# Kernel optimization log

Hardware: AMD Instinct MI355X
Metric: run time of the kernel (lower is better)

Reference implementation:

```python
import jax, jax.numpy as jnp
import numpy as np

N_QUBITS = 4
N_LAYERS = 3
H_IMG = 512

# ---------- 4-qubit statevector simulator, batched over P patches ----------

def _apply_1q(psi, U, w):
    # shared 2x2 gate U on wire w; psi: (P,2,2,2,2)
    psi = jnp.moveaxis(psi, 1 + w, -1)
    psi = jnp.einsum('ij,...j->...i', U, psi)
    return jnp.moveaxis(psi, -1, 1 + w)

def _apply_1q_batched(psi, U, w):
    # per-patch gate U: (P,2,2)
    psi = jnp.moveaxis(psi, 1 + w, -1)
    psi = jnp.einsum('pij,p...j->p...i', U, psi)
    return jnp.moveaxis(psi, -1, 1 + w)

def _apply_cnot(psi, c, t):
    psi = jnp.moveaxis(psi, (1 + c, 1 + t), (-2, -1))
    top = psi[..., 0:1, :]
    bot = psi[..., 1:2, ::-1]  # X on target when control=1
    psi = jnp.concatenate([top, bot], axis=-2)
    return jnp.moveaxis(psi, (-2, -1), (1 + c, 1 + t))

def _rx(theta):
    # AngleEmbedding default rotation='X'; theta: (P,) -> (P,2,2)
    h = theta * 0.5
    c = jnp.cos(h).astype(jnp.complex64)
    s = (-1j * jnp.sin(h)).astype(jnp.complex64)
    return jnp.stack([jnp.stack([c, s], -1), jnp.stack([s, c], -1)], -2)

def _rot(phi, theta, omega):
    # PennyLane Rot = RZ(omega) RY(theta) RZ(phi)
    c = jnp.cos(theta * 0.5)
    s = jnp.sin(theta * 0.5)
    em = jnp.exp(-0.5j * (phi + omega))
    ep = jnp.exp(0.5j * (phi + omega))
    fm = jnp.exp(0.5j * (phi - omega))
    fp = jnp.exp(-0.5j * (phi - omega))
    row0 = jnp.stack([em * c, -fm * s])
    row1 = jnp.stack([fp * s, ep * c])
    return jnp.stack([row0, row1]).astype(jnp.complex64)

def _qsim(inputs, weights):
    # inputs: (P,4) angles; weights: (3,4,3) Rot params -> (P,4) PauliZ expvals
    P = inputs.shape[0]
    psi = jnp.zeros((P, 2, 2, 2, 2), jnp.complex64).at[:, 0, 0, 0, 0].set(1.0)
    for w in range(N_QUBITS):
        psi = _apply_1q_batched(psi, _rx(inputs[:, w]), w)
    for l in range(N_LAYERS):
        for w in range(N_QUBITS):
            psi = _apply_1q(psi, _rot(weights[l, w, 0], weights[l, w, 1], weights[l, w, 2]), w)
        r = (l % (N_QUBITS - 1)) + 1  # StronglyEntanglingLayers default ranges
        for w in range(N_QUBITS):
            psi = _apply_cnot(psi, w, (w + r) % N_QUBITS)
    probs = psi.real ** 2 + psi.imag ** 2  # (P,2,2,2,2)
    ez = []
    for w in range(N_QUBITS):
        axes = tuple(a for a in range(1, 5) if a != 1 + w)
        p = probs.sum(axes)  # (P,2)
        ez.append(p[:, 0] - p[:, 1])
    return jnp.stack(ez, -1)  # (P,4)

def _qconv(x, q_weights):
    img = x[0, 0]  # (H,W)
    a = img[:-1, :-1]; b = img[:-1, 1:]; c = img[1:, :-1]; d = img[1:, 1:]
    Hm, Wm = a.shape
    patches = jnp.stack([a, b, c, d], -1).reshape(-1, 4)  # row-major 2x2 flatten
    ez = _qsim(patches, q_weights)  # (P,4)
    return ez.reshape(Hm, Wm, 4).transpose(2, 0, 1)[None]  # (1,4,Hm,Wm)

# ---------- classical layers ----------

def _conv(x, w, b):
    y = jax.lax.conv_general_dilated(x, w, (1, 1), 'VALID',
                                     dimension_numbers=('NCHW', 'OIHW', 'NCHW'))
    return y + b[None, :, None, None]

def _maxpool2(x):
    return jax.lax.reduce_window(x, -jnp.inf, jax.lax.max,
                                 (1, 1, 2, 2), (1, 1, 2, 2), 'VALID')

def _adaptive_max(x, out):
    H, W = x.shape[-2], x.shape[-1]
    rows = []
    for i in range(out):
        si, ei = (i * H) // out, -(-((i + 1) * H) // out)
        cols = []
        for j in range(out):
            sj, ej = (j * W) // out, -(-((j + 1) * W) // out)
            cols.append(x[..., si:ei, sj:ej].max((-2, -1)))
        rows.append(jnp.stack(cols, -1))
    return jnp.stack(rows, -2)


def setup_inputs() -> dict:
    key = jax.random.key(0)
    ks = jax.random.split(key, 10)
    x = jax.random.normal(ks[0], (1, 1, H_IMG, H_IMG), jnp.float32)
    q_weights = jax.random.uniform(ks[1], (N_LAYERS, N_QUBITS, 3), jnp.float32,
                                   0.0, 2.0 * np.pi)
    conv2_w = jax.random.normal(ks[2], (20, 4, 5, 5), jnp.float32) * 0.05
    conv2_b = jax.random.normal(ks[3], (20,), jnp.float32) * 0.05
    conv3_w = jax.random.normal(ks[4], (40, 20, 3, 3), jnp.float32) * 0.05
    conv3_b = jax.random.normal(ks[5], (40,), jnp.float32) * 0.05
    fc1_w = jax.random.normal(ks[6], (64, 640), jnp.float32) * 0.05
    fc1_b = jax.random.normal(ks[7], (64,), jnp.float32) * 0.05
    fc2_w = jax.random.normal(ks[8], (10, 64), jnp.float32) * 0.05
    fc2_b = jax.random.normal(ks[9], (10,), jnp.float32) * 0.05
    return {'x': x, 'q_weights': q_weights,
            'conv2_w': conv2_w, 'conv2_b': conv2_b,
            'conv3_w': conv3_w, 'conv3_b': conv3_b,
            'fc1_w': fc1_w, 'fc1_b': fc1_b,
            'fc2_w': fc2_w, 'fc2_b': fc2_b}


def reference(x, q_weights, conv2_w, conv2_b, conv3_w, conv3_b,
              fc1_w, fc1_b, fc2_w, fc2_b):
    h = _maxpool2(jax.nn.sigmoid(_qconv(x, q_weights)))        # (1,4,255,255)
    h = _maxpool2(jax.nn.relu(_conv(h, conv2_w, conv2_b)))      # (1,20,125,125)
    h = _adaptive_max(jax.nn.relu(_conv(h, conv3_w, conv3_b)), 4)  # (1,40,4,4)
    h = h.reshape(-1, 640)
    h = jax.nn.relu(h @ fc1_w.T + fc1_b)
    return h @ fc2_w.T + fc2_b  # (1,10)
```

## Files before the change

kernel.cpp:

```cpp
#include <hip/hip_runtime.h>
#include <math.h>

#define IMG 512
#define QO  255
#define QP  256
#define C2H 125
#define C2S 128
#define C3H 123
#define C3S 128

template<int M_>
__device__ inline void rot_regs(float2* a, float2 U00, float2 U01, float2 U10, float2 U11) {
    #pragma unroll
    for (int s = 0; s < 16; ++s) {
        if (!(s & M_)) {
            float2 a0 = a[s], a1 = a[s | M_];
            a[s]      = make_float2(U00.x*a0.x - U00.y*a0.y + U01.x*a1.x - U01.y*a1.y,
                                    U00.x*a0.y + U00.y*a0.x + U01.x*a1.y + U01.y*a1.x);
            a[s | M_] = make_float2(U10.x*a0.x - U10.y*a0.y + U11.x*a1.x - U11.y*a1.y,
                                    U10.x*a0.y + U10.y*a0.x + U11.x*a1.y + U11.y*a1.x);
        }
    }
}
template<int MC, int MT>
__device__ inline void cnot_regs(float2* a) {
    #pragma unroll
    for (int s = 0; s < 16; ++s) {
        if ((s & MC) && !(s & MT)) {
            float2 t = a[s]; a[s] = a[s | MT]; a[s | MT] = t;
        }
    }
}
__device__ inline void rot_gate_params(float phi, float th, float om,
                                       float2& U00, float2& U01, float2& U10, float2& U11) {
    float ch, sh, ca, sa, cb, sb;
    __sincosf(0.5f * th, &sh, &ch);
    __sincosf(0.5f * (phi + om), &sa, &ca);
    __sincosf(0.5f * (phi - om), &sb, &cb);
    U00 = make_float2( ca*ch, -sa*ch);
    U01 = make_float2(-cb*sh, -sb*sh);
    U10 = make_float2( cb*sh, -sb*sh);
    U11 = make_float2( ca*ch,  sa*ch);
}

__global__ void build_M(const float* __restrict__ qw, float2* __restrict__ Mout) {
    int t = threadIdx.x;
    if (t >= 16) return;
    float2 a[16];
    #pragma unroll
    for (int s = 0; s < 16; ++s) a[s] = make_float2(s == t ? 1.f : 0.f, 0.f);

    float2 U00, U01, U10, U11;
#define ROTG(L, W) rot_gate_params(qw[((L)*4+(W))*3+0], qw[((L)*4+(W))*3+1], qw[((L)*4+(W))*3+2], U00,U01,U10,U11); \
                   rot_regs<(1 << (3-(W)))>(a, U00, U01, U10, U11);
    ROTG(0,0) ROTG(0,1) ROTG(0,2) ROTG(0,3)
    cnot_regs<8,4>(a); cnot_regs<4,2>(a); cnot_regs<2,1>(a); cnot_regs<1,8>(a);
    ROTG(1,0) ROTG(1,1) ROTG(1,2) ROTG(1,3)
    cnot_regs<8,2>(a); cnot_regs<4,1>(a); cnot_regs<2,8>(a); cnot_regs<1,4>(a);
    ROTG(2,0) ROTG(2,1) ROTG(2,2) ROTG(2,3)
    cnot_regs<8,1>(a); cnot_regs<4,8>(a); cnot_regs<2,4>(a); cnot_regs<1,2>(a);
#undef ROTG

    int pc = __popc(t) & 3;
    #pragma unroll
    for (int row = 0; row < 16; ++row) {
        float2 v = a[row], o;
        if      (pc == 0) o = v;
        else if (pc == 1) o = make_float2( v.y, -v.x);
        else if (pc == 2) o = make_float2(-v.x, -v.y);
        else              o = make_float2(-v.y,  v.x);
        Mout[row * 16 + t] = o;
    }
}

__global__ __launch_bounds__(256) void qconv_pool(const float* __restrict__ img,
                                                  const float2* __restrict__ M2,
                                                  float* __restrict__ out) {
    int gid = blockIdx.x * 256 + threadIdx.x;
    if (gid >= QO * QO) return;
    int i = gid / QO, j = gid - i * QO;
    int r0 = 2 * i, c0 = 2 * j;

    float cs[3][3], sn[3][3];
    #pragma unroll
    for (int rr = 0; rr < 3; ++rr)
        #pragma unroll
        for (int cc = 0; cc < 3; ++cc) {
            float v = img[(r0 + rr) * IMG + c0 + cc];
            __sincosf(0.5f * v, &sn[rr][cc], &cs[rr][cc]);
        }

    float mx0 = -1e30f, mx1 = -1e30f, mx2 = -1e30f, mx3 = -1e30f;

    #pragma unroll
    for (int pr = 0; pr < 2; ++pr) {
        #pragma unroll
        for (int pc = 0; pc < 2; ++pc) {
            float c0v = cs[pr][pc],     s0 = sn[pr][pc];
            float c1v = cs[pr][pc+1],   s1 = sn[pr][pc+1];
            float c2v = cs[pr+1][pc],   s2 = sn[pr+1][pc];
            float c3v = cs[pr+1][pc+1], s3 = sn[pr+1][pc+1];
            float t01[4] = {c0v*c1v, c0v*s1, s0*c1v, s0*s1};
            float t23[4] = {c2v*c3v, c2v*s3, s2*c3v, s2*s3};
            float a[16];
            #pragma unroll
            for (int k = 0; k < 16; ++k) a[k] = t01[k >> 2] * t23[k & 3];

            float e0 = 0.f, e1 = 0.f, e2 = 0.f, e3 = 0.f;
            #pragma unroll 4
            for (int rw = 0; rw < 16; ++rw) {
                float re = 0.f, im = 0.f;
                #pragma unroll
                for (int k = 0; k < 16; ++k) {
                    float2 m = M2[rw * 16 + k];
                    re = fmaf(m.x, a[k], re);
                    im = fmaf(m.y, a[k], im);
                }
                float pp = fmaf(re, re, im * im);
                e0 += (rw & 8) ? -pp : pp;
                e1 += (rw & 4) ? -pp : pp;
                e2 += (rw & 2) ? -pp : pp;
                e3 += (rw & 1) ? -pp : pp;
            }
            mx0 = fmaxf(mx0, e0);
            mx1 = fmaxf(mx1, e1);
            mx2 = fmaxf(mx2, e2);
            mx3 = fmaxf(mx3, e3);
        }
    }

    int o = i * QP + j;
    out[0 * QP * QP + o] = 1.f / (1.f + __expf(-mx0));
    out[1 * QP * QP + o] = 1.f / (1.f + __expf(-mx1));
    out[2 * QP * QP + o] = 1.f / (1.f + __expf(-mx2));
    out[3 * QP * QP + o] = 1.f / (1.f + __expf(-mx3));
}

__global__ __launch_bounds__(256) void conv2_pool(const float* __restrict__ in,
                                                  const float* __restrict__ w,
                                                  const float* __restrict__ b,
                                                  float* __restrict__ out) {
    int oc = blockIdx.y;
    int sp = blockIdx.x * 256 + threadIdx.x;
    if (sp >= C2H * C2H) return;
    int i = sp / C2H, j = sp - i * C2H;
    const float* wb = w + oc * 100;

    float a00 = 0.f, a01 = 0.f, a10 = 0.f, a11 = 0.f;
    #pragma unroll
    for (int ic = 0; ic < 4; ++ic) {
        const float* ip = in + ic * QP * QP + (2 * i) * QP + 2 * j;
        float win[6][6];
        #pragma unroll
        for (int y = 0; y < 6; ++y) {
            #pragma unroll
            for (int h = 0; h < 3; ++h) {
                float2 v = *(const float2*)(ip + y * QP + 2 * h);
                win[y][2*h]   = v.x;
                win[y][2*h+1] = v.y;
            }
        }
        #pragma unroll
        for (int ky = 0; ky < 5; ++ky) {
            #pragma unroll
            for (int kx = 0; kx < 5; ++kx) {
                float wv = wb[ic * 25 + ky * 5 + kx];
                a00 = fmaf(win[ky][kx],     wv, a00);
                a01 = fmaf(win[ky][kx+1],   wv, a01);
                a10 = fmaf(win[ky+1][kx],   wv, a10);
                a11 = fmaf(win[ky+1][kx+1], wv, a11);
            }
        }
    }
    float m = fmaxf(fmaxf(a00, a01), fmaxf(a10, a11));
    out[oc * C2H * C2S + i * C2S + j] = fmaxf(m + b[oc], 0.f);
}

__global__ __launch_bounds__(256) void conv3_k(const float* __restrict__ in,
                                               const float* __restrict__ w,
                                               const float* __restrict__ b,
                                               float* __restrict__ out) {
    int og = blockIdx.y;
    int sp = blockIdx.x * 256 + threadIdx.x;
    if (sp >= C3H * C3H) return;
    int y = sp / C3H, x = sp - y * C3H;
    int oc0 = og * 4;
    const float* wb = w + oc0 * 180;

    float acc0 = 0.f, acc1 = 0.f, acc2 = 0.f, acc3 = 0.f;
    #pragma unroll
    for (int ic = 0; ic < 20; ++ic) {
        const float* ip = in + ic * C2H * C2S + y * C2S + x;
        float v[3][3];
        #pragma unroll
        for (int ky = 0; ky < 3; ++ky)
            #pragma unroll
            for (int kx = 0; kx < 3; ++kx)
                v[ky][kx] = ip[ky * C2S + kx];
        #pragma unroll
        for (int kk = 0; kk < 9; ++kk) {
            float iv = v[kk / 3][kk % 3];
            acc0 = fmaf(iv, wb[          ic * 9 + kk], acc0);
            acc1 = fmaf(iv, wb[180     + ic * 9 + kk], acc1);
            acc2 = fmaf(iv, wb[360     + ic * 9 + kk], acc2);
            acc3 = fmaf(iv, wb[540     + ic * 9 + kk], acc3);
        }
    }
    int o = y * C3S + x;
    out[(oc0 + 0) * C3H * C3S + o] = fmaxf(acc0 + b[oc0 + 0], 0.f);
    out[(oc0 + 1) * C3H * C3S + o] = fmaxf(acc1 + b[oc0 + 1], 0.f);
    out[(oc0 + 2) * C3H * C3S + o] = fmaxf(acc2 + b[oc0 + 2], 0.f);
    out[(oc0 + 3) * C3H * C3S + o] = fmaxf(acc3 + b[oc0 + 3], 0.f);
}

__global__ void amax_k(const float* __restrict__ in, float* __restrict__ out) {
    int ob = blockIdx.x;
    int oc = ob >> 4, bi = (ob >> 2) & 3, bj = ob & 3;
    int y0 = (bi * C3H) >> 2, y1 = ((bi + 1) * C3H + 3) >> 2;
    int x0 = (bj * C3H) >> 2, x1 = ((bj + 1) * C3H + 3) >> 2;
    int ny = y1 - y0, nx = x1 - x0, tot = ny * nx;
    float m = -1e30f;
    for (int e = threadIdx.x; e < tot; e += 64) {
        int yy = e / nx, xx = e - yy * nx;
        m = fmaxf(m, in[oc * C3H * C3S + (y0 + yy) * C3S + x0 + xx]);
    }
    #pragma unroll
    for (int o = 32; o > 0; o >>= 1) m = fmaxf(m, __shfl_down(m, o, 64));
    if (threadIdx.x == 0) out[ob] = m;
}

__global__ void fc_k(const float* __restrict__ h, const float* __restrict__ w1,
                     const float* __restrict__ b1, const float* __restrict__ w2,
                     const float* __restrict__ b2, float* __restrict__ out) {
    __shared__ float hh[640];
    __shared__ float h1[64];
    int t = threadIdx.x;
    for (int e = t; e < 640; e += 256) hh[e] = h[e];
    __syncthreads();

    int r = t >> 2, q = t & 3;
    const float4* wr = (const float4*)(w1 + r * 640 + q * 160);
    const float*  hp = hh + q * 160;
    float acc = 0.f;
    #pragma unroll 4
    for (int n = 0; n < 40; ++n) {
        float4 wv = wr[n];
        acc = fmaf(wv.x, hp[n*4+0], acc);
        acc = fmaf(wv.y, hp[n*4+1], acc);
        acc = fmaf(wv.z, hp[n*4+2], acc);
        acc = fmaf(wv.w, hp[n*4+3], acc);
    }
    acc += __shfl_xor(acc, 1, 64);
    acc += __shfl_xor(acc, 2, 64);
    if (q == 0) h1[r] = fmaxf(acc + b1[r], 0.f);
    __syncthreads();

    if (t < 10) {
        float o = b2[t];
        #pragma unroll 8
        for (int n = 0; n < 64; ++n) o = fmaf(h1[n], w2[t * 64 + n], o);
        out[t] = o;
    }
}

extern "C" void kernel_launch(void* const* d_in, const int* in_sizes, int n_in,
                              void* d_out, int out_size, void* d_ws, size_t ws_size,
                              hipStream_t stream) {
    const float* x   = (const float*)d_in[0];
    const float* qw  = (const float*)d_in[1];
    const float* c2w = (const float*)d_in[2];
    const float* c2b = (const float*)d_in[3];
    const float* c3w = (const float*)d_in[4];
    const float* c3b = (const float*)d_in[5];
    const float* f1w = (const float*)d_in[6];
    const float* f1b = (const float*)d_in[7];
    const float* f2w = (const float*)d_in[8];
    const float* f2b = (const float*)d_in[9];
    float* out = (float*)d_out;

    float*  wsf   = (float*)d_ws;
    float2* M     = (float2*)d_ws;
    float*  qout  = wsf + 512;
    float*  c2out = qout + 4 * QP * QP;
    float*  c3out = c2out + 20 * C2H * C2S;
    float*  am    = c3out + 40 * C3H * C3S;

    build_M<<<1, 64, 0, stream>>>(qw, M);
    qconv_pool<<<(QO * QO + 255) / 256, 256, 0, stream>>>(x, M, qout);
    conv2_pool<<<dim3((C2H * C2H + 255) / 256, 20), 256, 0, stream>>>(qout, c2w, c2b, c2out);
    conv3_k<<<dim3((C3H * C3H + 255) / 256, 10), 256, 0, stream>>>(c2out, c3w, c3b, c3out);
    amax_k<<<640, 64, 0, stream>>>(c3out, am);
    fc_k<<<1, 256, 0, stream>>>(am, f1w, f1b, f2w, f2b, out);
}
```

Baseline: 137.7 us.

## Fuse gate-matrix build into qconv, fuse adaptive max into conv3, split pool rows

The 16x16 circuit matrix is now built per block into shared memory inside qconv_pool, which removes the separate build_M launch and the global reads of M. Each pooled qconv output is now computed by two threads, one per pooling row, combined with a lane shuffle. That doubles parallelism and lowers per-thread work. The adaptive max pool is fused into conv3 using shared and global integer atomicMax on non-negative floats, so the conv3 output is never written to memory and the amax launch goes away. The cost is redundant matrix construction in every block, extra atomics, and zeroing of the pooled buffer inside conv2.

```diff
diff --git a/kernel.cpp b/kernel.cpp
--- a/kernel.cpp
+++ b/kernel.cpp
@@ -7,7 +7,6 @@
 #define C2H 125
 #define C2S 128
 #define C3H 123
-#define C3S 128
 
 template<int M_>
 __device__ inline void rot_regs(float2* a, float2 U00, float2 U01, float2 U10, float2 U11) {
@@ -43,47 +42,48 @@
     U11 = make_float2( ca*ch,  sa*ch);
 }
 
-__global__ void build_M(const float* __restrict__ qw, float2* __restrict__ Mout) {
-    int t = threadIdx.x;
-    if (t >= 16) return;
-    float2 a[16];
-    #pragma unroll
-    for (int s = 0; s < 16; ++s) a[s] = make_float2(s == t ? 1.f : 0.f, 0.f);
-
-    float2 U00, U01, U10, U11;
+__global__ __launch_bounds__(256) void qconv_pool(const float* __restrict__ img,
+                                                  const float* __restrict__ qw,
+                                                  float* __restrict__ out) {
+    __shared__ float2 Ms[256];
+    int tid = threadIdx.x;
+
+    if (tid < 16) {
+        float2 a[16];
+        #pragma unroll
+        for (int s = 0; s < 16; ++s) a[s] = make_float2(s == tid ? 1.f : 0.f, 0.f);
+        float2 U00, U01, U10, U11;
 #define ROTG(L, W) rot_gate_params(qw[((L)*4+(W))*3+0], qw[((L)*4+(W))*3+1], qw[((L)*4+(W))*3+2], U00,U01,U10,U11); \
                    rot_regs<(1 << (3-(W)))>(a, U00, U01, U10, U11);
-    ROTG(0,0) ROTG(0,1) ROTG(0,2) ROTG(0,3)
-    cnot_regs<8,4>(a); cnot_regs<4,2>(a); cnot_regs<2,1>(a); cnot_regs<1,8>(a);
-    ROTG(1,0) ROTG(1,1) ROTG(1,2) ROTG(1,3)
-    cnot_regs<8,2>(a); cnot_regs<4,1>(a); cnot_regs<2,8>(a); cnot_regs<1,4>(a);
-    ROTG(2,0) ROTG(2,1) ROTG(2,2) ROTG(2,3)
-    cnot_regs<8,1>(a); cnot_regs<4,8>(a); cnot_regs<2,4>(a); cnot_regs<1,2>(a);
+        ROTG(0,0) ROTG(0,1) ROTG(0,2) ROTG(0,3)
+        cnot_regs<8,4>(a); cnot_regs<4,2>(a); cnot_regs<2,1>(a); cnot_regs<1,8>(a);
+        ROTG(1,0) ROTG(1,1) ROTG(1,2) ROTG(1,3)
+        cnot_regs<8,2>(a); cnot_regs<4,1>(a); cnot_regs<2,8>(a); cnot_regs<1,4>(a);
+        ROTG(2,0) ROTG(2,1) ROTG(2,2) ROTG(2,3)
+        cnot_regs<8,1>(a); cnot_regs<4,8>(a); cnot_regs<2,4>(a); cnot_regs<1,2>(a);
 #undef ROTG
-
-    int pc = __popc(t) & 3;
-    #pragma unroll
-    for (int row = 0; row < 16; ++row) {
-        float2 v = a[row], o;
-        if      (pc == 0) o = v;
-        else if (pc == 1) o = make_float2( v.y, -v.x);
-        else if (pc == 2) o = make_float2(-v.x, -v.y);
-        else              o = make_float2(-v.y,  v.x);
-        Mout[row * 16 + t] = o;
-    }
-}
-
-__global__ __launch_bounds__(256) void qconv_pool(const float* __restrict__ img,
-                                                  const float2* __restrict__ M2,
-                                                  float* __restrict__ out) {
-    int gid = blockIdx.x * 256 + threadIdx.x;
-    if (gid >= QO * QO) return;
-    int i = gid / QO, j = gid - i * QO;
-    int r0 = 2 * i, c0 = 2 * j;
-
-    float cs[3][3], sn[3][3];
-    #pragma unroll
-    for (int rr = 0; rr < 3; ++rr)
+        int pc4 = __popc(tid) & 3;
+        #pragma unroll
+        for (int row = 0; row < 16; ++row) {
+            float2 v = a[row], o;
+            if      (pc4 == 0) o = v;
+            else if (pc4 == 1) o = make_float2( v.y, -v.x);
+            else if (pc4 == 2) o = make_float2(-v.x, -v.y);
+            else               o = make_float2(-v.y,  v.x);
+            Ms[row * 16 + tid] = o;
+        }
+    }
+    __syncthreads();
+
+    int gid = blockIdx.x * 256 + tid;
+    int pid = gid >> 1, p = gid & 1;
+    if (pid >= QO * QO) return;
+    int i = pid / QO, j = pid - i * QO;
+    int r0 = 2 * i + p, c0 = 2 * j;
+
+    float cs[2][3], sn[2][3];
+    #pragma unroll
+    for (int rr = 0; rr < 2; ++rr)
         #pragma unroll
         for (int cc = 0; cc < 3; ++cc) {
             float v = img[(r0 + rr) * IMG + c0 + cc];
@@ -93,53 +93,61 @@
     float mx0 = -1e30f, mx1 = -1e30f, mx2 = -1e30f, mx3 = -1e30f;
 
     #pragma unroll
-    for (int pr = 0; pr < 2; ++pr) {
-        #pragma unroll
-        for (int pc = 0; pc < 2; ++pc) {
-            float c0v = cs[pr][pc],     s0 = sn[pr][pc];
-            float c1v = cs[pr][pc+1],   s1 = sn[pr][pc+1];
-            float c2v = cs[pr+1][pc],   s2 = sn[pr+1][pc];
-            float c3v = cs[pr+1][pc+1], s3 = sn[pr+1][pc+1];
-            float t01[4] = {c0v*c1v, c0v*s1, s0*c1v, s0*s1};
-            float t23[4] = {c2v*c3v, c2v*s3, s2*c3v, s2*s3};
-            float a[16];
-            #pragma unroll
-            for (int k = 0; k < 16; ++k) a[k] = t01[k >> 2] * t23[k & 3];
-
-            float e0 = 0.f, e1 = 0.f, e2 = 0.f, e3 = 0.f;
-            #pragma unroll 4
-            for (int rw = 0; rw < 16; ++rw) {
-                float re = 0.f, im = 0.f;
-                #pragma unroll
-                for (int k = 0; k < 16; ++k) {
-                    float2 m = M2[rw * 16 + k];
-                    re = fmaf(m.x, a[k], re);
-                    im = fmaf(m.y, a[k], im);
-                }
-                float pp = fmaf(re, re, im * im);
-                e0 += (rw & 8) ? -pp : pp;
-                e1 += (rw & 4) ? -pp : pp;
-                e2 += (rw & 2) ? -pp : pp;
-                e3 += (rw & 1) ? -pp : pp;
-            }
-            mx0 = fmaxf(mx0, e0);
-            mx1 = fmaxf(mx1, e1);
-            mx2 = fmaxf(mx2, e2);
-            mx3 = fmaxf(mx3, e3);
-        }
-    }
-
-    int o = i * QP + j;
-    out[0 * QP * QP + o] = 1.f / (1.f + __expf(-mx0));
-    out[1 * QP * QP + o] = 1.f / (1.f + __expf(-mx1));
-    out[2 * QP * QP + o] = 1.f / (1.f + __expf(-mx2));
-    out[3 * QP * QP + o] = 1.f / (1.f + __expf(-mx3));
+    for (int pc = 0; pc < 2; ++pc) {
+        float c0v = cs[0][pc],   s0 = sn[0][pc];
+        float c1v = cs[0][pc+1], s1 = sn[0][pc+1];
+        float c2v = cs[1][pc],   s2 = sn[1][pc];
+        float c3v = cs[1][pc+1], s3 = sn[1][pc+1];
+        float t01[4] = {c0v*c1v, c0v*s1, s0*c1v, s0*s1};
+        float t23[4] = {c2v*c3v, c2v*s3, s2*c3v, s2*s3};
+        float a[16];
+        #pragma unroll
+        for (int k = 0; k < 16; ++k) a[k] = t01[k >> 2] * t23[k & 3];
+
+        float e0 = 0.f, e1 = 0.f, e2 = 0.f, e3 = 0.f;
+        #pragma unroll 4
+        for (int rw = 0; rw < 16; ++rw) {
+            float re = 0.f, im = 0.f;
+            #pragma unroll
+            for (int k = 0; k < 16; ++k) {
+                float2 m = Ms[rw * 16 + k];
+                re = fmaf(m.x, a[k], re);
+                im = fmaf(m.y, a[k], im);
+            }
+            float pp = fmaf(re, re, im * im);
+            e0 += (rw & 8) ? -pp : pp;
+            e1 += (rw & 4) ? -pp : pp;
+            e2 += (rw & 2) ? -pp : pp;
+            e3 += (rw & 1) ? -pp : pp;
+        }
+        mx0 = fmaxf(mx0, e0);
+        mx1 = fmaxf(mx1, e1);
+        mx2 = fmaxf(mx2, e2);
+        mx3 = fmaxf(mx3, e3);
+    }
+
+    mx0 = fmaxf(mx0, __shfl_xor(mx0, 1, 64));
+    mx1 = fmaxf(mx1, __shfl_xor(mx1, 1, 64));
+    mx2 = fmaxf(mx2, __shfl_xor(mx2, 1, 64));
+    mx3 = fmaxf(mx3, __shfl_xor(mx3, 1, 64));
+
+    if (p == 0) {
+        int o = i * QP + j;
+        out[0 * QP * QP + o] = 1.f / (1.f + __expf(-mx0));
+        out[1 * QP * QP + o] = 1.f / (1.f + __expf(-mx1));
+        out[2 * QP * QP + o] = 1.f / (1.f + __expf(-mx2));
+        out[3 * QP * QP + o] = 1.f / (1.f + __expf(-mx3));
+    }
 }
 
 __global__ __launch_bounds__(256) void conv2_pool(const float* __restrict__ in,
                                                   const float* __restrict__ w,
                                                   const float* __restrict__ b,
-                                                  float* __restrict__ out) {
+                                                  float* __restrict__ out,
+                                                  float* __restrict__ am) {
+    if (blockIdx.x == 0 && blockIdx.y == 0) {
+        for (int e = threadIdx.x; e < 640; e += 256) am[e] = 0.f;
+    }
     int oc = blockIdx.y;
     int sp = blockIdx.x * 256 + threadIdx.x;
     if (sp >= C2H * C2H) return;
@@ -176,57 +184,68 @@
     out[oc * C2H * C2S + i * C2S + j] = fmaxf(m + b[oc], 0.f);
 }
 
-__global__ __launch_bounds__(256) void conv3_k(const float* __restrict__ in,
-                                               const float* __restrict__ w,
-                                               const float* __restrict__ b,
-                                               float* __restrict__ out) {
-    int og = blockIdx.y;
+__global__ __launch_bounds__(256) void conv3_amax(const float* __restrict__ in,
+                                                  const float* __restrict__ w,
+                                                  const float* __restrict__ b,
+                                                  int* __restrict__ am) {
+    __shared__ int bm[64];
+    int og = blockIdx.y, oc0 = og * 4;
+    if (threadIdx.x < 64) bm[threadIdx.x] = 0;
+    __syncthreads();
+
     int sp = blockIdx.x * 256 + threadIdx.x;
-    if (sp >= C3H * C3H) return;
-    int y = sp / C3H, x = sp - y * C3H;
-    int oc0 = og * 4;
-    const float* wb = w + oc0 * 180;
-
-    float acc0 = 0.f, acc1 = 0.f, acc2 = 0.f, acc3 = 0.f;
-    #pragma unroll
-    for (int ic = 0; ic < 20; ++ic) {
-        const float* ip = in + ic * C2H * C2S + y * C2S + x;
-        float v[3][3];
-        #pragma unroll
-        for (int ky = 0; ky < 3; ++ky)
-            #pragma unroll
-            for (int kx = 0; kx < 3; ++kx)
-                v[ky][kx] = ip[ky * C2S + kx];
-        #pragma unroll
-        for (int kk = 0; kk < 9; ++kk) {
-            float iv = v[kk / 3][kk % 3];
-            acc0 = fmaf(iv, wb[          ic * 9 + kk], acc0);
-            acc1 = fmaf(iv, wb[180     + ic * 9 + kk], acc1);
-            acc2 = fmaf(iv, wb[360     + ic * 9 + kk], acc2);
-            acc3 = fmaf(iv, wb[540     + ic * 9 + kk], acc3);
-        }
-    }
-    int o = y * C3S + x;
-    out[(oc0 + 0) * C3H * C3S + o] = fmaxf(acc0 + b[oc0 + 0], 0.f);
-    out[(oc0 + 1) * C3H * C3S + o] = fmaxf(acc1 + b[oc0 + 1], 0.f);
-    out[(oc0 + 2) * C3H * C3S + o] = fmaxf(acc2 + b[oc0 + 2], 0.f);
-    out[(oc0 + 3) * C3H * C3S + o] = fmaxf(acc3 + b[oc0 + 3], 0.f);
-}
-
-__global__ void amax_k(const float* __restrict__ in, float* __restrict__ out) {
-    int ob = blockIdx.x;
-    int oc = ob >> 4, bi = (ob >> 2) & 3, bj = ob & 3;
-    int y0 = (bi * C3H) >> 2, y1 = ((bi + 1) * C3H + 3) >> 2;
-    int x0 = (bj * C3H) >> 2, x1 = ((bj + 1) * C3H + 3) >> 2;
-    int ny = y1 - y0, nx = x1 - x0, tot = ny * nx;
-    float m = -1e30f;
-    for (int e = threadIdx.x; e < tot; e += 64) {
-        int yy = e / nx, xx = e - yy * nx;
-        m = fmaxf(m, in[oc * C3H * C3S + (y0 + yy) * C3S + x0 + xx]);
-    }
-    #pragma unroll
-    for (int o = 32; o > 0; o >>= 1) m = fmaxf(m, __shfl_down(m, o, 64));
-    if (threadIdx.x == 0) out[ob] = m;
+    if (sp < C3H * C3H) {
+        int y = sp / C3H, x = sp - y * C3H;
+        const float* wb = w + oc0 * 180;
+
+        float acc0 = 0.f, acc1 = 0.f, acc2 = 0.f, acc3 = 0.f;
+        #pragma unroll
+        for (int ic = 0; ic < 20; ++ic) {
+            const float* ip = in + ic * C2H * C2S + y * C2S + x;
+            float v[3][3];
+            #pragma unroll
+            for (int ky = 0; ky < 3; ++ky)
+                #pragma unroll
+                for (int kx = 0; kx < 3; ++kx)
+                    v[ky][kx] = ip[ky * C2S + kx];
+            #pragma unroll
+            for (int kk = 0; kk < 9; ++kk) {
+                float iv = v[kk / 3][kk % 3];
+                acc0 = fmaf(iv, wb[      ic * 9 + kk], acc0);
+                acc1 = fmaf(iv, wb[180 + ic * 9 + kk], acc1);
+                acc2 = fmaf(iv, wb[360 + ic * 9 + kk], acc2);
+                acc3 = fmaf(iv, wb[540 + ic * 9 + kk], acc3);
+            }
+        }
+        acc0 = fmaxf(acc0 + b[oc0 + 0], 0.f);
+        acc1 = fmaxf(acc1 + b[oc0 + 1], 0.f);
+        acc2 = fmaxf(acc2 + b[oc0 + 2], 0.f);
+        acc3 = fmaxf(acc3 + b[oc0 + 3], 0.f);
+
+        const int bs[4] = {0, 30, 61, 92};
+        const int be[4] = {31, 62, 93, 123};
+        #pragma unroll
+        for (int yb = 0; yb < 4; ++yb) {
+            if (y >= bs[yb] && y < be[yb]) {
+                #pragma unroll
+                for (int xb = 0; xb < 4; ++xb) {
+                    if (x >= bs[xb] && x < be[xb]) {
+                        int bin = yb * 4 + xb;
+                        atomicMax(&bm[0 * 16 + bin], __float_as_int(acc0));
+                        atomicMax(&bm[1 * 16 + bin], __float_as_int(acc1));
+                        atomicMax(&bm[2 * 16 + bin], __float_as_int(acc2));
+                        atomicMax(&bm[3 * 16 + bin], __float_as_int(acc3));
+                    }
+                }
+            }
+        }
+    }
+    __syncthreads();
+    if (threadIdx.x < 64) {
+        int v = bm[threadIdx.x];
+        if (v != 0)
+            atomicMax(&am[(oc0 + (threadIdx.x >> 4)) * 16 + (threadIdx.x & 15)], v);
+    }
 }
 
 __global__ void fc_k(const float* __restrict__ h, const float* __restrict__ w1,
@@ -278,17 +297,13 @@
     const float* f2b = (const float*)d_in[9];
     float* out = (float*)d_out;
 
-    float*  wsf   = (float*)d_ws;
-    float2* M     = (float2*)d_ws;
-    float*  qout  = wsf + 512;
-    float*  c2out = qout + 4 * QP * QP;
-    float*  c3out = c2out + 20 * C2H * C2S;
-    float*  am    = c3out + 40 * C3H * C3S;
-
-    build_M<<<1, 64, 0, stream>>>(qw, M);
-    qconv_pool<<<(QO * QO + 255) / 256, 256, 0, stream>>>(x, M, qout);
-    conv2_pool<<<dim3((C2H * C2H + 255) / 256, 20), 256, 0, stream>>>(qout, c2w, c2b, c2out);
-    conv3_k<<<dim3((C3H * C3H + 255) / 256, 10), 256, 0, stream>>>(c2out, c3w, c3b, c3out);
-    amax_k<<<640, 64, 0, stream>>>(c3out, am);
+    float* wsf   = (float*)d_ws;
+    float* qout  = wsf;
+    float* c2out = qout + 4 * QP * QP;
+    float* am    = c2out + 20 * C2H * C2S;
+
+    qconv_pool<<<(2 * QO * QO + 255) / 256, 256, 0, stream>>>(x, qw, qout);
+    conv2_pool<<<dim3((C2H * C2H + 255) / 256, 20), 256, 0, stream>>>(qout, c2w, c2b, c2out, am);
+    conv3_amax<<<dim3((C3H * C3H + 255) / 256, 10), 256, 0, stream>>>(c2out, c3w, c3b, (int*)am);
     fc_k<<<1, 256, 0, stream>>>(am, f1w, f1b, f2w, f2b, out);
 }
```

Result: slower. 142.3 us (+3.4%).
